# Optimization experiments

Measured on AMD Instinct MI355X. Metric: run time of the kernel, lower is better.

## Reference

```python
import jax, jax.numpy as jnp
import numpy as np

B, T = 8192, 4096
N_GROUPS = 64
SIZES = np.tile(np.array([32, 64, 96, 64], dtype=np.int32), 16)
SEG_IDS = np.repeat(np.arange(N_GROUPS, dtype=np.int32), SIZES)  # [T]


def setup_inputs() -> dict:
    key = jax.random.key(0)
    k1, k2, k3 = jax.random.split(key, 3)
    H = jax.random.normal(k1, (B, T), dtype=jnp.float32)
    # nn.Linear(hidden_dim=1, 1): weight [1,1], bias [1]
    score_w = jax.random.normal(k2, (1, 1), dtype=jnp.float32)
    score_b = jax.random.normal(k3, (1,), dtype=jnp.float32) * 0.1
    return {"H": H, "score_w": score_w, "score_b": score_b}


def reference(H, score_w, score_b):
    seg_ids = jnp.asarray(SEG_IDS)
    sizes = jnp.asarray(SIZES, dtype=H.dtype)  # [G]
    # ragged segment mean over the feature axis: G[b,g] = mean(H[b, sl_g])
    G = jax.ops.segment_sum(H.T, seg_ids, num_segments=N_GROUPS).T / sizes  # [B, G]
    # score = Linear(1,1) applied to G.unsqueeze(-1), then squeeze -> affine on G
    scores = G * score_w[0, 0] + score_b[0]  # [B, G]
    a = jax.nn.softmax(scores, axis=1)  # [B, G]
    Z = jnp.sum(a * G, axis=1)  # [B]
    return Z, a
```

## Files before the change

kernel.cpp:

```cpp
#include <hip/hip_runtime.h>


#define TPB 256

__global__ __launch_bounds__(TPB) void agp_kernel(
    const float* __restrict__ H,
    const float* __restrict__ score_w,
    const float* __restrict__ score_b,
    float* __restrict__ Z,
    float* __restrict__ A,
    int T)
{
  const int b    = blockIdx.x;
  const int tid  = threadIdx.x;
  const int lane = tid & 63;
  const int w    = tid >> 6;
  const float4* row = (const float4*)(H + (size_t)b * T);

  __shared__ float groups[64];

  float4 v0 = row[tid];
  float4 v1 = row[tid + TPB];
  float4 v2 = row[tid + 2 * TPB];
  float4 v3 = row[tid + 3 * TPB];

  float s[4];
  s[0] = (v0.x + v0.y) + (v0.z + v0.w);
  s[1] = (v1.x + v1.y) + (v1.z + v1.w);
  s[2] = (v2.x + v2.y) + (v2.z + v2.w);
  s[3] = (v3.x + v3.y) + (v3.z + v3.w);

  const float invsz[4] = {1.f / 32.f, 1.f / 64.f, 1.f / 96.f, 1.f / 64.f};

#pragma unroll
  for (int k = 0; k < 4; ++k) {
    float os = s[k];
    os += __shfl_xor(os, 1);
    os += __shfl_xor(os, 2);
    os += __shfl_xor(os, 4);

    const float o0 = __shfl(os, 0);
    const float o1 = __shfl(os, 8);
    const float o2 = __shfl(os, 16);
    const float o3 = __shfl(os, 24);
    const float o4 = __shfl(os, 32);
    const float o5 = __shfl(os, 40);
    const float o6 = __shfl(os, 48);
    const float o7 = __shfl(os, 56);

    const int c = w + 4 * k;
    if (lane < 4) {
      float g = (lane == 0) ? o0
              : (lane == 1) ? (o1 + o2)
              : (lane == 2) ? ((o3 + o4) + o5)
                            : (o6 + o7);
      groups[4 * c + lane] = g * invsz[lane];
    }
  }
  __syncthreads();

  if (tid < 64) {
    const float G = groups[tid];
    const float score = G * score_w[0] + score_b[0];

    float m = score;
#pragma unroll
    for (int mask = 32; mask >= 1; mask >>= 1)
      m = fmaxf(m, __shfl_xor(m, mask));

    const float e = __expf(score - m);
    float se = e;
    float sg = e * G;
#pragma unroll
    for (int mask = 32; mask >= 1; mask >>= 1) {
      se += __shfl_xor(se, mask);
      sg += __shfl_xor(sg, mask);
    }

    A[(size_t)b * 64 + tid] = e / se;
    if (tid == 0) Z[b] = sg / se;
  }
}

extern "C" void kernel_launch(void* const* d_in, const int* in_sizes, int n_in,
                              void* d_out, int out_size, void* d_ws, size_t ws_size,
                              hipStream_t stream) {
  const float* H  = (const float*)d_in[0];
  const float* sw = (const float*)d_in[1];
  const float* sb = (const float*)d_in[2];

  const int T = 4096;
  const int B = in_sizes[0] / T;

  float* Z = (float*)d_out;
  float* A = Z + B;

  agp_kernel<<<B, TPB, 0, stream>>>(H, sw, sb, Z, A, T);
}
```

Before: 190.3 us.

## Process eight rows per block with register double-buffered prefetch of next row

```diff
diff --git a/kernel.cpp b/kernel.cpp
--- a/kernel.cpp
+++ b/kernel.cpp
@@ -2,83 +2,100 @@
 
 
 #define TPB 256
+#define RPB 8
 
 __global__ __launch_bounds__(TPB) void agp_kernel(
     const float* __restrict__ H,
     const float* __restrict__ score_w,
     const float* __restrict__ score_b,
     float* __restrict__ Z,
-    float* __restrict__ A,
-    int T)
+    float* __restrict__ A)
 {
-  const int b    = blockIdx.x;
   const int tid  = threadIdx.x;
   const int lane = tid & 63;
   const int w    = tid >> 6;
-  const float4* row = (const float4*)(H + (size_t)b * T);
 
-  __shared__ float groups[64];
+  __shared__ float groups[2][64];
 
-  float4 v0 = row[tid];
-  float4 v1 = row[tid + TPB];
-  float4 v2 = row[tid + 2 * TPB];
-  float4 v3 = row[tid + 3 * TPB];
+  const float sw = score_w[0];
+  const float sb = score_b[0];
 
-  float s[4];
-  s[0] = (v0.x + v0.y) + (v0.z + v0.w);
-  s[1] = (v1.x + v1.y) + (v1.z + v1.w);
-  s[2] = (v2.x + v2.y) + (v2.z + v2.w);
-  s[3] = (v3.x + v3.y) + (v3.z + v3.w);
+  const int row0 = blockIdx.x * RPB;
+  const float4* p = (const float4*)H + (size_t)row0 * 1024;
+
+  float4 cv0 = p[tid];
+  float4 cv1 = p[tid + 256];
+  float4 cv2 = p[tid + 512];
+  float4 cv3 = p[tid + 768];
 
   const float invsz[4] = {1.f / 32.f, 1.f / 64.f, 1.f / 96.f, 1.f / 64.f};
 
-#pragma unroll
-  for (int k = 0; k < 4; ++k) {
-    float os = s[k];
-    os += __shfl_xor(os, 1);
-    os += __shfl_xor(os, 2);
-    os += __shfl_xor(os, 4);
-
-    const float o0 = __shfl(os, 0);
-    const float o1 = __shfl(os, 8);
-    const float o2 = __shfl(os, 16);
-    const float o3 = __shfl(os, 24);
-    const float o4 = __shfl(os, 32);
-    const float o5 = __shfl(os, 40);
-    const float o6 = __shfl(os, 48);
-    const float o7 = __shfl(os, 56);
-
-    const int c = w + 4 * k;
-    if (lane < 4) {
-      float g = (lane == 0) ? o0
-              : (lane == 1) ? (o1 + o2)
-              : (lane == 2) ? ((o3 + o4) + o5)
-                            : (o6 + o7);
-      groups[4 * c + lane] = g * invsz[lane];
-    }
-  }
-  __syncthreads();
-
-  if (tid < 64) {
-    const float G = groups[tid];
-    const float score = G * score_w[0] + score_b[0];
-
-    float m = score;
-#pragma unroll
-    for (int mask = 32; mask >= 1; mask >>= 1)
-      m = fmaxf(m, __shfl_xor(m, mask));
-
-    const float e = __expf(score - m);
-    float se = e;
-    float sg = e * G;
-#pragma unroll
-    for (int mask = 32; mask >= 1; mask >>= 1) {
-      se += __shfl_xor(se, mask);
-      sg += __shfl_xor(sg, mask);
+  for (int r = 0; r < RPB; ++r) {
+    float4 nv0, nv1, nv2, nv3;
+    if (r + 1 < RPB) {
+      const float4* pn = p + (size_t)(r + 1) * 1024;
+      nv0 = pn[tid];
+      nv1 = pn[tid + 256];
+      nv2 = pn[tid + 512];
+      nv3 = pn[tid + 768];
     }
 
-    A[(size_t)b * 64 + tid] = e / se;
-    if (tid == 0) Z[b] = sg / se;
+    float s[4];
+    s[0] = (cv0.x + cv0.y) + (cv0.z + cv0.w);
+    s[1] = (cv1.x + cv1.y) + (cv1.z + cv1.w);
+    s[2] = (cv2.x + cv2.y) + (cv2.z + cv2.w);
+    s[3] = (cv3.x + cv3.y) + (cv3.z + cv3.w);
+
+#pragma unroll
+    for (int k = 0; k < 4; ++k) {
+      float os = s[k];
+      os += __shfl_xor(os, 1);
+      os += __shfl_xor(os, 2);
+      os += __shfl_xor(os, 4);
+
+      const float o0 = __shfl(os, 0);
+      const float o1 = __shfl(os, 8);
+      const float o2 = __shfl(os, 16);
+      const float o3 = __shfl(os, 24);
+      const float o4 = __shfl(os, 32);
+      const float o5 = __shfl(os, 40);
+      const float o6 = __shfl(os, 48);
+      const float o7 = __shfl(os, 56);
+
+      const int c = w + 4 * k;
+      if (lane < 4) {
+        float g = (lane == 0) ? o0
+                : (lane == 1) ? (o1 + o2)
+                : (lane == 2) ? ((o3 + o4) + o5)
+                              : (o6 + o7);
+        groups[r & 1][4 * c + lane] = g * invsz[lane];
+      }
+    }
+    __syncthreads();
+
+    if (tid < 64) {
+      const float G = groups[r & 1][tid];
+      const float score = G * sw + sb;
+
+      float m = score;
+#pragma unroll
+      for (int mask = 32; mask >= 1; mask >>= 1)
+        m = fmaxf(m, __shfl_xor(m, mask));
+
+      const float e = __expf(score - m);
+      float se = e;
+      float sg = e * G;
+#pragma unroll
+      for (int mask = 32; mask >= 1; mask >>= 1) {
+        se += __shfl_xor(se, mask);
+        sg += __shfl_xor(sg, mask);
+      }
+
+      A[(size_t)(row0 + r) * 64 + tid] = e / se;
+      if (tid == 0) Z[row0 + r] = sg / se;
+    }
+
+    if (r + 1 < RPB) { cv0 = nv0; cv1 = nv1; cv2 = nv2; cv3 = nv3; }
   }
 }
 
@@ -95,5 +112,5 @@
   float* Z = (float*)d_out;
   float* A = Z + B;
 
-  agp_kernel<<<B, TPB, 0, stream>>>(H, sw, sb, Z, A, T);
+  agp_kernel<<<B / RPB, TPB, 0, stream>>>(H, sw, sb, Z, A);
 }
```

Result: slower. 198.4 us (+4.2%).
